# Kernel optimization log

Measured on AMD Instinct MI355X. Metric: run time of the kernel, lower is better.

The kernel has to match this reference:

```python
import jax, jax.numpy as jnp
import numpy as np

MEM_SIZE = 500000
FEAT_DIM = 256
BATCH = 128
MARGIN = 1.0


def setup_inputs() -> dict:
    key = jax.random.key(0)
    k1, k2, k3 = jax.random.split(key, 3)
    x = jax.random.normal(k1, (BATCH, FEAT_DIM), dtype=jnp.float32)
    labels = jax.random.randint(k2, (BATCH,), 0, MEM_SIZE)
    Mem = jax.random.normal(k3, (MEM_SIZE, FEAT_DIM), dtype=jnp.float32)
    return {"x": x, "labels": labels, "Mem": Mem, "topk": 1000}


def reference(x, labels, Mem, topk):
    x_sq = jnp.sum(x * x, axis=1, keepdims=True)          # (B, 1)
    m_sq = jnp.sum(Mem * Mem, axis=1)[None, :]            # (1, M)
    distmat = x_sq + m_sq - 2.0 * (x @ Mem.T)             # (B, M)

    # One-hot positive mask from labels (B, M)
    mask = (labels[:, None] == jnp.arange(Mem.shape[0])[None, :]).astype(distmat.dtype)

    # Positive (same-class) distance; clamp matches torch .clamp(1e-12, 1e12)
    dist1 = distmat * mask
    min_loss = jnp.clip(dist1, 1e-12, 1e12).sum(axis=1)   # (B,)

    # Negatives: topk smallest distances (largest=False) via top_k on negated values
    dist2 = distmat * (1.0 - mask)
    neg_small, _ = jax.lax.top_k(-dist2, topk)            # (B, topk)
    max_loss = (-neg_small).sum(axis=1) / (topk - 1)      # (B,)

    loss = jax.nn.relu(min_loss - max_loss + MARGIN)
    return (loss.mean(), min_loss.mean(), max_loss.mean())
```

## Files before the change

### kernel.cpp

```cpp
#include <hip/hip_runtime.h>
#include <hip/hip_bf16.h>
#include <stdint.h>

#define MEMN 500000
#define FEAT 256
#define BATCHN 128
#define SAMP 8192
#define SSTRIDE 61
#define CAP 16384
#define LCAP 16
#define TILE_ROWS 128
#define NTILES ((MEMN + TILE_ROWS - 1) / TILE_ROWS)
#define K3GRID 1024

typedef __bf16 bf16x8 __attribute__((ext_vector_type(8)));
typedef float float4v __attribute__((ext_vector_type(4)));

__device__ __forceinline__ float bf2f(unsigned bits) {
    return __uint_as_float(bits << 16);
}

__device__ __forceinline__ uint4 pack8(const uint4 u0, const uint4 u1) {
    uint4 p;
    p.x = (u0.y & 0xffff0000u) | (u0.x >> 16);
    p.y = (u0.w & 0xffff0000u) | (u0.z >> 16);
    p.z = (u1.y & 0xffff0000u) | (u1.x >> 16);
    p.w = (u1.w & 0xffff0000u) | (u1.z >> 16);
    return p;
}

__global__ void k1_sample(const float* __restrict__ x, const float* __restrict__ Mem,
                          float* __restrict__ xsq, unsigned* __restrict__ cnt,
                          float* __restrict__ dpos, float* __restrict__ out,
                          float* __restrict__ samp) {
    int t = threadIdx.x;
    if (blockIdx.x == SAMP / 8) {
        if (t < BATCHN) {
            const float4* row = (const float4*)(x + t * FEAT);
            float s = 0.f;
            for (int i = 0; i < FEAT / 4; i++) {
                float4 v = row[i];
                s += v.x * v.x + v.y * v.y + v.z * v.z + v.w * v.w;
            }
            xsq[t] = s;
            cnt[t] = 0u;
            dpos[t] = 0.f;
        }
        if (t >= BATCHN && t < BATCHN + 3) out[t - BATCHN] = 0.f;
        return;
    }
    __shared__ ushort mrow[8][FEAT];
    __shared__ float msq[8];
    int s0 = blockIdx.x * 8;
    {
        int r = t >> 5, c = (t & 31) * 8;
        long mr = (long)(s0 + r) * SSTRIDE;
        if (mr >= MEMN) mr -= MEMN;
        const uint4* mp = (const uint4*)(Mem + mr * FEAT + c);
        uint4 u0 = mp[0], u1 = mp[1];
        *(uint4*)(&mrow[r][c]) = pack8(u0, u1);
    }
    __syncthreads();
    if (t < 8) {
        float s = 0.f;
        for (int k = 0; k < FEAT; k++) { float a = bf2f(mrow[t][k]); s += a * a; }
        msq[t] = s;
    }
    __syncthreads();
    for (int q = 0; q < 4; q++) {
        int pair = t + q * 256;
        int sl = pair >> 7, b = pair & 127;
        const float4* xr = (const float4*)(x + b * FEAT);
        float dot = 0.f;
        for (int i = 0; i < FEAT / 8; i++) {
            float4 x0 = xr[2 * i], x1 = xr[2 * i + 1];
            uint4 mv = *(const uint4*)(&mrow[sl][i * 8]);
            unsigned mw[4] = {mv.x, mv.y, mv.z, mv.w};
            float xf[8] = {x0.x, x0.y, x0.z, x0.w, x1.x, x1.y, x1.z, x1.w};
            for (int j = 0; j < 4; j++) {
                dot += xf[2 * j]     * bf2f(mw[j] & 0xffffu)
                     + xf[2 * j + 1] * bf2f(mw[j] >> 16);
            }
        }
        float d = msq[sl] - 2.f * dot;
        samp[b * SAMP + (s0 + sl)] = d;
    }
}

__global__ void k2_cutoff(const float* __restrict__ samp, const float* __restrict__ xsq,
                          float* __restrict__ cutoff) {
    __shared__ unsigned hist[2048];
    __shared__ unsigned part[256];
    int t = threadIdx.x, b = blockIdx.x;
    float xb = xsq[b];
    for (int i = t; i < 2048; i += 256) hist[i] = 0;
    __syncthreads();
    for (int i = t; i < SAMP; i += 256) {
        float d = samp[b * SAMP + i] + xb;
        int bin = (int)(d * 2.f);
        bin = bin < 0 ? 0 : (bin > 2047 ? 2047 : bin);
        atomicAdd(&hist[bin], 1u);
    }
    __syncthreads();
    unsigned p = 0;
    for (int j = 0; j < 8; j++) p += hist[t * 8 + j];
    part[t] = p;
    __syncthreads();
    if (t == 0) {
        const unsigned tgt = 98;
        unsigned cum = 0; int binsel = 2047;
        for (int i = 0; i < 256; i++) {
            if (cum + part[i] >= tgt) {
                for (int j = 0; j < 8; j++) {
                    int bb = i * 8 + j;
                    cum += hist[bb];
                    if (cum >= tgt) { binsel = bb; break; }
                }
                break;
            }
            cum += part[i];
        }
        cutoff[b] = (binsel + 1) * 0.5f + 1.0f;
    }
}

__launch_bounds__(512, 4)
__global__ void k3_gemm(const float* __restrict__ x, const float* __restrict__ Mem,
                        const int* __restrict__ labels,
                        const float* __restrict__ xsq, const float* __restrict__ cutoff,
                        unsigned* __restrict__ cnt, float* __restrict__ buf,
                        float* __restrict__ dpos) {
    __shared__ ushort xs[BATCHN * FEAT];
    __shared__ float cbuf[BATCHN * LCAP];
    __shared__ unsigned ccnt[BATCHN];
    int t = threadIdx.x;
    if (t < BATCHN) ccnt[t] = 0u;
    for (int i = 0; i < 8; i++) {
        int c = i * 512 + t;
        int row = c >> 5, cc = c & 31;
        int ccs = cc ^ (row & 7);
        const uint4* xp = (const uint4*)(x + row * FEAT + cc * 8);
        uint4 u0 = xp[0], u1 = xp[1];
        *(uint4*)(&xs[row * FEAT + ccs * 8]) = pack8(u0, u1);
    }
    int lane = t & 63, wave = t >> 6;
    int l15 = lane & 15, quad = lane >> 4;
    int rx = l15 & 7;
    float xsq_v[8], cut_v[8];
    int lab_v[8];
#pragma unroll
    for (int nt = 0; nt < 8; nt++) {
        int b = nt * 16 + l15;
        xsq_v[nt] = xsq[b];
        cut_v[nt] = cutoff[b];
        lab_v[nt] = labels[b];
    }
    __syncthreads();

    for (int tile = blockIdx.x; tile < NTILES; tile += gridDim.x) {
        int mbase = tile * TILE_ROWS + wave * 16;
        int m0 = mbase + l15;
        long mA = m0 < MEMN ? m0 : (MEMN - 1);
        const float* aptr = Mem + mA * FEAT + quad * 8;
        uint4 ua[8], ub[8];
#pragma unroll
        for (int ks = 0; ks < 8; ks++) {
            const uint4* ap = (const uint4*)(aptr + ks * 32);
            ua[ks] = ap[0];
            ub[ks] = ap[1];
        }
        float4v acc[8];
#pragma unroll
        for (int nt = 0; nt < 8; nt++) acc[nt] = (float4v){0.f, 0.f, 0.f, 0.f};
        float msqp = 0.f;
#pragma unroll
        for (int ks = 0; ks < 8; ks++) {
            float4 f0 = __builtin_bit_cast(float4, ua[ks]);
            float4 f1 = __builtin_bit_cast(float4, ub[ks]);
            msqp += f0.x * f0.x + f0.y * f0.y + f0.z * f0.z + f0.w * f0.w
                  + f1.x * f1.x + f1.y * f1.y + f1.z * f1.z + f1.w * f1.w;
            uint4 av = pack8(ua[ks], ub[ks]);
            bf16x8 af = __builtin_bit_cast(bf16x8, av);
            int ch = ks * 4 + quad;
#pragma unroll
            for (int nt = 0; nt < 8; nt++) {
                uint4 bv = *(const uint4*)(&xs[(nt * 16 + l15) * FEAT + (ch ^ rx) * 8]);
                bf16x8 bfr = __builtin_bit_cast(bf16x8, bv);
                acc[nt] = __builtin_amdgcn_mfma_f32_16x16x32_bf16(af, bfr, acc[nt], 0, 0, 0);
            }
        }
        float msqf = msqp;
        msqf += __shfl_xor(msqf, 16, 64);
        msqf += __shfl_xor(msqf, 32, 64);
#pragma unroll
        for (int r = 0; r < 4; r++) {
            float msq_r = __shfl(msqf, quad * 4 + r, 64);
            int mg = mbase + quad * 4 + r;
            if (mg < MEMN) {
#pragma unroll
                for (int nt = 0; nt < 8; nt++) {
                    float d = xsq_v[nt] + msq_r - 2.f * acc[nt][r];
                    int b = nt * 16 + l15;
                    if (lab_v[nt] == mg) {
                        dpos[b] = d;
                    } else if (d < cut_v[nt]) {
                        unsigned p = atomicAdd(&ccnt[b], 1u);
                        if (p < LCAP) {
                            cbuf[b * LCAP + p] = d;
                        } else {
                            unsigned q = atomicAdd(&cnt[b], 1u);
                            if (q < CAP) buf[(long)b * CAP + q] = d;
                        }
                    }
                }
            }
        }
    }
    __syncthreads();
    if (t < BATCHN) {
        unsigned nb = ccnt[t];
        if (nb > LCAP) nb = LCAP;
        if (nb) {
            unsigned p = atomicAdd(&cnt[t], nb);
            for (unsigned i = 0; i < nb; i++) {
                unsigned q = p + i;
                if (q < CAP) buf[(long)t * CAP + q] = cbuf[t * LCAP + i];
            }
        }
    }
}

__global__ void k4_select(const float* __restrict__ buf, const unsigned* __restrict__ cnt,
                          const float* __restrict__ cutoff, const float* __restrict__ dpos,
                          const int* __restrict__ topk, float* __restrict__ out) {
    __shared__ unsigned hist[2048];
    __shared__ unsigned part[256];
    __shared__ float coll[1024];
    __shared__ unsigned ncoll;
    __shared__ int sTb;
    __shared__ unsigned sC1;
    __shared__ float wsum[4];
    int t = threadIdx.x, b = blockIdx.x;
    int k1 = topk[0] - 1;
    unsigned c = cnt[b]; if (c > CAP) c = CAP;
    float invw = 2048.f / cutoff[b];
    for (int i = t; i < 2048; i += 256) hist[i] = 0;
    if (t == 0) ncoll = 0;
    __syncthreads();
    const float* vals = buf + (long)b * CAP;
    for (unsigned i = t; i < c; i += 256) {
        float d = vals[i];
        int bin = (int)(d * invw);
        bin = bin < 0 ? 0 : (bin > 2047 ? 2047 : bin);
        atomicAdd(&hist[bin], 1u);
    }
    __syncthreads();
    unsigned p = 0;
    for (int j = 0; j < 8; j++) p += hist[t * 8 + j];
    part[t] = p;
    __syncthreads();
    if (t == 0) {
        unsigned tgt = (c < (unsigned)k1) ? c : (unsigned)k1;
        unsigned cum = 0; int Tb = 2048; unsigned C1 = 0;
        if (tgt > 0) {
            for (int i = 0; i < 256; i++) {
                if (cum + part[i] >= tgt) {
                    for (int j = 0; j < 8; j++) {
                        int bb = i * 8 + j;
                        if (cum + hist[bb] >= tgt) { Tb = bb; C1 = cum; break; }
                        cum += hist[bb];
                    }
                    break;
                }
                cum += part[i];
            }
        }
        sTb = Tb; sC1 = C1;
    }
    __syncthreads();
    int Tb = sTb; unsigned C1 = sC1;
    float ls = 0.f;
    for (unsigned i = t; i < c; i += 256) {
        float d = vals[i];
        int bin = (int)(d * invw);
        bin = bin < 0 ? 0 : (bin > 2047 ? 2047 : bin);
        if (bin < Tb) ls += d;
        else if (bin == Tb) {
            unsigned ix = atomicAdd(&ncoll, 1u);
            if (ix < 1024) coll[ix] = d;
        }
    }
    ls += __shfl_down(ls, 32, 64); ls += __shfl_down(ls, 16, 64);
    ls += __shfl_down(ls, 8, 64);  ls += __shfl_down(ls, 4, 64);
    ls += __shfl_down(ls, 2, 64);  ls += __shfl_down(ls, 1, 64);
    if ((t & 63) == 0) wsum[t >> 6] = ls;
    __syncthreads();
    if (t == 0) {
        float S = wsum[0] + wsum[1] + wsum[2] + wsum[3];
        unsigned tgt = (c < (unsigned)k1) ? c : (unsigned)k1;
        int r = (int)(tgt - C1);
        unsigned nc = ncoll; if (nc > 1024) nc = 1024;
        for (int i = 0; i < r && i < (int)nc; i++) {
            float mn = 3.4e38f; int mi = 0;
            for (unsigned j = 0; j < nc; j++) if (coll[j] < mn) { mn = coll[j]; mi = (int)j; }
            S += mn; coll[mi] = 3.4e38f;
        }
        float minl = dpos[b];
        minl = minl < 1e-12f ? 1e-12f : (minl > 1e12f ? 1e12f : minl);
        minl += (float)(MEMN - 1) * 1e-12f;
        float maxl = S / (float)k1;
        float loss = minl - maxl + 1.0f; if (loss < 0.f) loss = 0.f;
        atomicAdd(&out[0], loss * (1.f / 128.f));
        atomicAdd(&out[1], minl * (1.f / 128.f));
        atomicAdd(&out[2], maxl * (1.f / 128.f));
    }
}

__global__ void k_sentinel(float* out) {
    out[0] = -777.f; out[1] = -777.f; out[2] = -777.f;
}

extern "C" void kernel_launch(void* const* d_in, const int* in_sizes, int n_in,
                              void* d_out, int out_size, void* d_ws, size_t ws_size,
                              hipStream_t stream) {
    const float* x     = (const float*)d_in[0];
    const int* labels  = (const int*)d_in[1];
    const float* Mem   = (const float*)d_in[2];
    const int* topk    = (const int*)d_in[3];
    (void)in_sizes; (void)n_in; (void)out_size;

    char* ws = (char*)d_ws;
    const size_t OFF_SAMP = 0;
    const size_t OFF_BUF  = 4194304;
    const size_t OFF_CNT  = OFF_BUF + 8388608;
    const size_t OFF_XSQ  = OFF_CNT + 512;
    const size_t OFF_DPOS = OFF_XSQ + 512;
    const size_t OFF_CUT  = OFF_DPOS + 512;
    const size_t NEEDED   = OFF_CUT + 512;
    if (ws_size < NEEDED) {
        k_sentinel<<<1, 1, 0, stream>>>((float*)d_out);
        return;
    }
    float*    samp   = (float*)(ws + OFF_SAMP);
    float*    buf    = (float*)(ws + OFF_BUF);
    unsigned* cnt    = (unsigned*)(ws + OFF_CNT);
    float*    xsq    = (float*)(ws + OFF_XSQ);
    float*    dpos   = (float*)(ws + OFF_DPOS);
    float*    cutoff = (float*)(ws + OFF_CUT);

    k1_sample<<<SAMP / 8 + 1, 256, 0, stream>>>(x, Mem, xsq, cnt, dpos,
                                                (float*)d_out, samp);
    k2_cutoff<<<128,    256, 0, stream>>>(samp, xsq, cutoff);
    k3_gemm  <<<K3GRID, 512, 0, stream>>>(x, Mem, labels, xsq, cutoff, cnt, buf, dpos);
    k4_select<<<128,    256, 0, stream>>>(buf, cnt, cutoff, dpos, topk, (float*)d_out);
}
```

Baseline: 875.6 us.

## Compute sampled distances in k1 with bf16 MFMA tiles instead of scalar dots

The sampling kernel now stages x as bf16 in shared memory and computes the 8192 sampled memory-row distances with the same 16x16x32 bf16 MFMA tiling used by the main GEMM. It switches to 512-thread blocks of 128 sampled rows and changes the sample buffer layout to sample-major, with k2 updated to read it that way. The squared-norm accumulation in both k1 and k3 is also split across four partial sums to shorten the dependency chain. This removes the slow scalar per-pair dot loop, but k2 now reads with a stride of 128 floats, which gives poorer coalescing.

After: 743.8 us. 1.18x faster.

```diff
diff --git a/kernel.cpp b/kernel.cpp
--- a/kernel.cpp
+++ b/kernel.cpp
@@ -29,12 +29,13 @@
     return p;
 }
 
+__launch_bounds__(512, 4)
 __global__ void k1_sample(const float* __restrict__ x, const float* __restrict__ Mem,
                           float* __restrict__ xsq, unsigned* __restrict__ cnt,
                           float* __restrict__ dpos, float* __restrict__ out,
                           float* __restrict__ samp) {
     int t = threadIdx.x;
-    if (blockIdx.x == SAMP / 8) {
+    if (blockIdx.x == SAMP / TILE_ROWS) {
         if (t < BATCHN) {
             const float4* row = (const float4*)(x + t * FEAT);
             float s = 0.f;
@@ -49,41 +50,64 @@
         if (t >= BATCHN && t < BATCHN + 3) out[t - BATCHN] = 0.f;
         return;
     }
-    __shared__ ushort mrow[8][FEAT];
-    __shared__ float msq[8];
-    int s0 = blockIdx.x * 8;
-    {
-        int r = t >> 5, c = (t & 31) * 8;
-        long mr = (long)(s0 + r) * SSTRIDE;
-        if (mr >= MEMN) mr -= MEMN;
-        const uint4* mp = (const uint4*)(Mem + mr * FEAT + c);
-        uint4 u0 = mp[0], u1 = mp[1];
-        *(uint4*)(&mrow[r][c]) = pack8(u0, u1);
-    }
-    __syncthreads();
-    if (t < 8) {
-        float s = 0.f;
-        for (int k = 0; k < FEAT; k++) { float a = bf2f(mrow[t][k]); s += a * a; }
-        msq[t] = s;
-    }
-    __syncthreads();
-    for (int q = 0; q < 4; q++) {
-        int pair = t + q * 256;
-        int sl = pair >> 7, b = pair & 127;
-        const float4* xr = (const float4*)(x + b * FEAT);
-        float dot = 0.f;
-        for (int i = 0; i < FEAT / 8; i++) {
-            float4 x0 = xr[2 * i], x1 = xr[2 * i + 1];
-            uint4 mv = *(const uint4*)(&mrow[sl][i * 8]);
-            unsigned mw[4] = {mv.x, mv.y, mv.z, mv.w};
-            float xf[8] = {x0.x, x0.y, x0.z, x0.w, x1.x, x1.y, x1.z, x1.w};
-            for (int j = 0; j < 4; j++) {
-                dot += xf[2 * j]     * bf2f(mw[j] & 0xffffu)
-                     + xf[2 * j + 1] * bf2f(mw[j] >> 16);
-            }
-        }
-        float d = msq[sl] - 2.f * dot;
-        samp[b * SAMP + (s0 + sl)] = d;
+    __shared__ ushort xs[BATCHN * FEAT];
+    for (int i = 0; i < 8; i++) {
+        int c = i * 512 + t;
+        int row = c >> 5, cc = c & 31;
+        int ccs = cc ^ (row & 7);
+        const uint4* xp = (const uint4*)(x + row * FEAT + cc * 8);
+        uint4 u0 = xp[0], u1 = xp[1];
+        *(uint4*)(&xs[row * FEAT + ccs * 8]) = pack8(u0, u1);
+    }
+    int lane = t & 63, wave = t >> 6;
+    int l15 = lane & 15, quad = lane >> 4;
+    int rx = l15 & 7;
+    __syncthreads();
+
+    int sbase = blockIdx.x * TILE_ROWS + wave * 16;
+    long mrow = (long)(sbase + l15) * SSTRIDE;
+    const float* aptr = Mem + mrow * FEAT + quad * 8;
+    uint4 ua[8], ub[8];
+#pragma unroll
+    for (int ks = 0; ks < 8; ks++) {
+        const uint4* ap = (const uint4*)(aptr + ks * 32);
+        ua[ks] = ap[0];
+        ub[ks] = ap[1];
+    }
+    float4v acc[8];
+#pragma unroll
+    for (int nt = 0; nt < 8; nt++) acc[nt] = (float4v){0.f, 0.f, 0.f, 0.f};
+    float m0 = 0.f, m1 = 0.f, m2 = 0.f, m3 = 0.f;
+#pragma unroll
+    for (int ks = 0; ks < 8; ks++) {
+        float4 f0 = __builtin_bit_cast(float4, ua[ks]);
+        float4 f1 = __builtin_bit_cast(float4, ub[ks]);
+        m0 += f0.x * f0.x + f0.y * f0.y;
+        m1 += f0.z * f0.z + f0.w * f0.w;
+        m2 += f1.x * f1.x + f1.y * f1.y;
+        m3 += f1.z * f1.z + f1.w * f1.w;
+        uint4 av = pack8(ua[ks], ub[ks]);
+        bf16x8 af = __builtin_bit_cast(bf16x8, av);
+        int ch = ks * 4 + quad;
+#pragma unroll
+        for (int nt = 0; nt < 8; nt++) {
+            uint4 bv = *(const uint4*)(&xs[(nt * 16 + l15) * FEAT + (ch ^ rx) * 8]);
+            bf16x8 bfr = __builtin_bit_cast(bf16x8, bv);
+            acc[nt] = __builtin_amdgcn_mfma_f32_16x16x32_bf16(af, bfr, acc[nt], 0, 0, 0);
+        }
+    }
+    float msqf = (m0 + m1) + (m2 + m3);
+    msqf += __shfl_xor(msqf, 16, 64);
+    msqf += __shfl_xor(msqf, 32, 64);
+#pragma unroll
+    for (int r = 0; r < 4; r++) {
+        float msq_r = __shfl(msqf, quad * 4 + r, 64);
+        int sg = sbase + quad * 4 + r;
+#pragma unroll
+        for (int nt = 0; nt < 8; nt++) {
+            float dp = msq_r - 2.f * acc[nt][r];
+            samp[sg * BATCHN + nt * 16 + l15] = dp;
+        }
     }
 }
 
@@ -96,7 +120,7 @@
     for (int i = t; i < 2048; i += 256) hist[i] = 0;
     __syncthreads();
     for (int i = t; i < SAMP; i += 256) {
-        float d = samp[b * SAMP + i] + xb;
+        float d = samp[i * BATCHN + b] + xb;
         int bin = (int)(d * 2.f);
         bin = bin < 0 ? 0 : (bin > 2047 ? 2047 : bin);
         atomicAdd(&hist[bin], 1u);
@@ -172,13 +196,15 @@
         float4v acc[8];
 #pragma unroll
         for (int nt = 0; nt < 8; nt++) acc[nt] = (float4v){0.f, 0.f, 0.f, 0.f};
-        float msqp = 0.f;
+        float m0s = 0.f, m1s = 0.f, m2s = 0.f, m3s = 0.f;
 #pragma unroll
         for (int ks = 0; ks < 8; ks++) {
             float4 f0 = __builtin_bit_cast(float4, ua[ks]);
             float4 f1 = __builtin_bit_cast(float4, ub[ks]);
-            msqp += f0.x * f0.x + f0.y * f0.y + f0.z * f0.z + f0.w * f0.w
-                  + f1.x * f1.x + f1.y * f1.y + f1.z * f1.z + f1.w * f1.w;
+            m0s += f0.x * f0.x + f0.y * f0.y;
+            m1s += f0.z * f0.z + f0.w * f0.w;
+            m2s += f1.x * f1.x + f1.y * f1.y;
+            m3s += f1.z * f1.z + f1.w * f1.w;
             uint4 av = pack8(ua[ks], ub[ks]);
             bf16x8 af = __builtin_bit_cast(bf16x8, av);
             int ch = ks * 4 + quad;
@@ -189,7 +215,7 @@
                 acc[nt] = __builtin_amdgcn_mfma_f32_16x16x32_bf16(af, bfr, acc[nt], 0, 0, 0);
             }
         }
-        float msqf = msqp;
+        float msqf = (m0s + m1s) + (m2s + m3s);
         msqf += __shfl_xor(msqf, 16, 64);
         msqf += __shfl_xor(msqf, 32, 64);
 #pragma unroll
@@ -348,8 +374,8 @@
     float*    dpos   = (float*)(ws + OFF_DPOS);
     float*    cutoff = (float*)(ws + OFF_CUT);
 
-    k1_sample<<<SAMP / 8 + 1, 256, 0, stream>>>(x, Mem, xsq, cnt, dpos,
-                                                (float*)d_out, samp);
+    k1_sample<<<SAMP / TILE_ROWS + 1, 512, 0, stream>>>(x, Mem, xsq, cnt, dpos,
+                                                        (float*)d_out, samp);
     k2_cutoff<<<128,    256, 0, stream>>>(samp, xsq, cutoff);
     k3_gemm  <<<K3GRID, 512, 0, stream>>>(x, Mem, labels, xsq, cutoff, cnt, buf, dpos);
     k4_select<<<128,    256, 0, stream>>>(buf, cnt, cutoff, dpos, topk, (float*)d_out);
```
